# Optimization experiments

Measured on AMD Instinct MI355X. Metric: run time of the kernel, lower is better.

The kernel has to match this reference:

```python
import jax, jax.numpy as jnp
import numpy as np

NUM_STEPS = 2  # consensus iterations


def psi3(r, edge_index, W3, b3):
    # one-layer message passing GNN: sum-aggregate neighbors, add self, linear, relu
    src, dst = edge_index[0], edge_index[1]
    agg = jnp.zeros_like(r).at[dst].add(r[src])
    return jax.nn.relu((r + agg) @ W3 + b3)


def setup_inputs() -> dict:
    key = jax.random.key(0)
    ks = jax.random.split(key, 12)
    N_total, C_in = 4096, 128   # global entity table
    N_s, N_t = 1024, 1024       # source / target graph sizes (B=1)
    E = 16384                   # edges per graph (avg degree 16)
    C1, C2 = 256, 256           # psi_1 / psi_2 output dims
    R = 32                      # psi_3 in_channels == out_channels
    s_in = 1.0 / np.sqrt(C_in)
    s_r = 1.0 / np.sqrt(R)
    inp = {}
    inp['inputs'] = jax.random.normal(ks[0], (N_total, C_in), jnp.float32)
    inp['index_n1'] = jax.random.randint(ks[1], (N_s,), 0, N_total)
    inp['index_n2'] = jax.random.randint(ks[2], (N_t,), 0, N_total)
    inp['edge_index_s'] = jax.random.randint(ks[3], (2, E), 0, N_s)
    inp['edge_index_t'] = jax.random.randint(ks[4], (2, E), 0, N_t)
    # psi_1 / psi_2: linear entity encoders
    inp['W1'] = jax.random.uniform(ks[5], (C_in, C1), jnp.float32, -s_in, s_in)
    inp['W2'] = jax.random.uniform(ks[6], (C_in, C2), jnp.float32, -s_in, s_in)
    # psi_3 weights
    inp['W3'] = jax.random.uniform(ks[7], (R, R), jnp.float32, -s_r, s_r)
    inp['b3'] = jnp.zeros((R,), jnp.float32)
    # consensus MLP: R -> R -> 1
    inp['Wm1'] = jax.random.uniform(ks[8], (R, R), jnp.float32, -s_r, s_r)
    inp['bm1'] = jnp.zeros((R,), jnp.float32)
    inp['Wm2'] = jax.random.uniform(ks[9], (R, 1), jnp.float32, -s_r, s_r)
    inp['bm2'] = jnp.zeros((1,), jnp.float32)
    # random node indicator functions r_s for each consensus step (drawn
    # with torch.randn inside the original forward; precomputed here)
    inp['rs_all'] = jax.random.normal(ks[10], (NUM_STEPS, N_s, R), jnp.float32)
    return inp


def reference(inputs, index_n1, index_n2, edge_index_s, edge_index_t,
              W1, W2, W3, b3, Wm1, bm1, Wm2, bm2, rs_all):
    time_emb = inputs @ W1  # psi_1
    rel_emb = inputs @ W2   # psi_2
    # h = cat(time, rel) per node; B=1 so masks are all-true
    h_s = jnp.concatenate([time_emb[index_n1], rel_emb[index_n1]], axis=-1)  # [N_s, C1+C2]
    h_t = jnp.concatenate([time_emb[index_n2], rel_emb[index_n2]], axis=-1)  # [N_t, C1+C2]
    S_hat = h_s @ h_t.T  # [N_s, N_t] dense similarity
    S_0 = jax.nn.softmax(S_hat, axis=-1)  # masked_softmax with full mask

    def step(S_hat, r_s):
        S = jax.nn.softmax(S_hat, axis=-1)
        r_t = S.T @ r_s                                  # [N_t, R]
        o_s = psi3(r_s, edge_index_s, W3, b3)            # [N_s, R]
        o_t = psi3(r_t, edge_index_t, W3, b3)            # [N_t, R]
        D = o_s[:, None, :] - o_t[None, :, :]            # [N_s, N_t, R]
        delta = (jax.nn.relu(D @ Wm1 + bm1) @ Wm2 + bm2)[..., 0]  # mlp(D).squeeze(-1)
        return S_hat + delta, None

    S_hat, _ = jax.lax.scan(step, S_hat, rs_all)
    S_L = jax.nn.softmax(S_hat, axis=-1)
    return S_0, S_L
```

## Files before the change

### kernel.cpp

```cpp
#include <hip/hip_runtime.h>
#include <math.h>

#define N_S   1024
#define N_T   1024
#define C_IN  128
#define E_EDG 16384
#define R     32
#define NSTEP 2

__global__ __launch_bounds__(128) void k_gram(const float* __restrict__ W1,
                                              const float* __restrict__ W2,
                                              float* __restrict__ G) {
    int a = blockIdx.x;
    int b = threadIdx.x;
    __shared__ float wa[512];
    for (int c = threadIdx.x; c < 256; c += 128) {
        wa[c]       = W1[a * 256 + c];
        wa[256 + c] = W2[a * 256 + c];
    }
    __syncthreads();
    float acc = 0.f;
    for (int c = 0; c < 256; ++c)
        acc += wa[c] * W1[b * 256 + c] + wa[256 + c] * W2[b * 256 + c];
    G[a * 128 + b] = acc;
}

__global__ __launch_bounds__(128) void k_ys(const float* __restrict__ X,
                                            const int* __restrict__ idx1,
                                            const float* __restrict__ G,
                                            float* __restrict__ Ys) {
    int i = blockIdx.x;
    int a = threadIdx.x;
    __shared__ float x[128];
    int row = idx1[i];
    x[a] = X[row * 128 + a];
    __syncthreads();
    float acc = 0.f;
#pragma unroll 8
    for (int d = 0; d < 128; ++d)
        acc += x[d] * G[d * 128 + a];
    Ys[i * 128 + a] = acc;
}

__global__ __launch_bounds__(256) void k_shat(const float* __restrict__ Ys,
                                              const float* __restrict__ X,
                                              const int* __restrict__ idx2,
                                              float* __restrict__ Shat) {
    __shared__ float As[64][132];
    __shared__ float Bs[64][132];
    const int i0 = blockIdx.y * 64, j0 = blockIdx.x * 64;
    const int t = threadIdx.x;
    for (int s = t; s < 64 * 32; s += 256) {
        int row = s >> 5, q = s & 31;
        float4 v = ((const float4*)(Ys + (size_t)(i0 + row) * 128))[q];
        *(float4*)&As[row][q * 4] = v;
    }
    for (int s = t; s < 64 * 32; s += 256) {
        int row = s >> 5, q = s & 31;
        int src = idx2[j0 + row];
        float4 v = ((const float4*)(X + (size_t)src * 128))[q];
        *(float4*)&Bs[row][q * 4] = v;
    }
    __syncthreads();
    const int r = t >> 4, c = t & 15;
    float acc[4][4] = {};
    for (int k = 0; k < 128; k += 4) {
        float4 ya[4], xb[4];
#pragma unroll
        for (int a = 0; a < 4; ++a) ya[a] = *(const float4*)&As[r + 16 * a][k];
#pragma unroll
        for (int b = 0; b < 4; ++b) xb[b] = *(const float4*)&Bs[c + 16 * b][k];
#pragma unroll
        for (int a = 0; a < 4; ++a)
#pragma unroll
            for (int b = 0; b < 4; ++b)
                acc[a][b] += ya[a].x * xb[b].x + ya[a].y * xb[b].y +
                             ya[a].z * xb[b].z + ya[a].w * xb[b].w;
    }
#pragma unroll
    for (int a = 0; a < 4; ++a)
#pragma unroll
        for (int b = 0; b < 4; ++b)
            Shat[(size_t)(i0 + r + 16 * a) * 1024 + (j0 + c + 16 * b)] = acc[a][b];
}

__global__ __launch_bounds__(256) void k_softmax(const float* __restrict__ Shat,
                                                 float* __restrict__ Sdst,
                                                 float* __restrict__ out0) {
    int i = blockIdx.x;
    int t = threadIdx.x;
    const float* row = Shat + (size_t)i * 1024;
    float x[4];
#pragma unroll
    for (int j = 0; j < 4; ++j) x[j] = row[t + 256 * j];
    __shared__ float red[256];
    float m = fmaxf(fmaxf(x[0], x[1]), fmaxf(x[2], x[3]));
    red[t] = m;
    __syncthreads();
    for (int s = 128; s > 0; s >>= 1) {
        if (t < s) red[t] = fmaxf(red[t], red[t + s]);
        __syncthreads();
    }
    float rowmax = red[0];
    __syncthreads();
    float e[4], sum = 0.f;
#pragma unroll
    for (int j = 0; j < 4; ++j) { e[j] = expf(x[j] - rowmax); sum += e[j]; }
    red[t] = sum;
    __syncthreads();
    for (int s = 128; s > 0; s >>= 1) {
        if (t < s) red[t] += red[t + s];
        __syncthreads();
    }
    float inv = 1.f / red[0];
#pragma unroll
    for (int j = 0; j < 4; ++j) {
        float v = e[j] * inv;
        Sdst[(size_t)i * 1024 + t + 256 * j] = v;
        if (out0) out0[(size_t)i * 1024 + t + 256 * j] = v;
    }
}

__global__ __launch_bounds__(256) void k_rt(const float* __restrict__ S,
                                            const float* __restrict__ rs,
                                            float* __restrict__ rt) {
    int j0 = blockIdx.x * 64;
    int i0 = blockIdx.y * 128;
    int t = threadIdx.x;
    int k = t & 31;
    int jg = t >> 5;
    __shared__ float Sl[16][68];
    __shared__ float Rl[16][36];
    float acc[8] = {};
    for (int ic = 0; ic < 128; ic += 16) {
        for (int s = t; s < 16 * 16; s += 256) {
            int row = s >> 4, q = s & 15;
            *(float4*)&Sl[row][q * 4] =
                ((const float4*)(S + (size_t)(i0 + ic + row) * 1024 + j0))[q];
        }
        for (int s = t; s < 16 * 8; s += 256) {
            int row = s >> 3, q = s & 7;
            *(float4*)&Rl[row][q * 4] =
                ((const float4*)(rs + (size_t)(i0 + ic + row) * 32))[q];
        }
        __syncthreads();
#pragma unroll
        for (int ii = 0; ii < 16; ++ii) {
            float rv = Rl[ii][k];
#pragma unroll
            for (int m = 0; m < 8; ++m)
                acc[m] += Sl[ii][jg * 8 + m] * rv;
        }
        __syncthreads();
    }
#pragma unroll
    for (int m = 0; m < 8; ++m)
        atomicAdd(&rt[(size_t)(j0 + jg * 8 + m) * 32 + k], acc[m]);
}

__global__ __launch_bounds__(256) void k_scatter(const int* __restrict__ es,
                                                 const int* __restrict__ et,
                                                 const float* __restrict__ rs,
                                                 const float* __restrict__ rt,
                                                 float* __restrict__ aggs,
                                                 float* __restrict__ aggt) {
    int gid = blockIdx.x * 256 + threadIdx.x;
    int k = gid & 31;
    int e = gid >> 5;
    if (e < E_EDG) {
        int src = es[e], dst = es[E_EDG + e];
        atomicAdd(&aggs[(size_t)dst * 32 + k], rs[(size_t)src * 32 + k]);
    } else {
        e -= E_EDG;
        int src = et[e], dst = et[E_EDG + e];
        atomicAdd(&aggt[(size_t)dst * 32 + k], rt[(size_t)src * 32 + k]);
    }
}

__global__ __launch_bounds__(256) void k_post(const float* __restrict__ rs,
                                              const float* __restrict__ rt,
                                              const float* __restrict__ aggs,
                                              const float* __restrict__ aggt,
                                              const float* __restrict__ W3,
                                              const float* __restrict__ b3,
                                              const float* __restrict__ Wm1,
                                              const float* __restrict__ bm1,
                                              float* __restrict__ P,
                                              float* __restrict__ Q) {
    __shared__ float w3[1024], wm1[1024];
    __shared__ float ul[8][33], ol[8][33];
    int t = threadIdx.x;
    for (int s = t; s < 1024; s += 256) { w3[s] = W3[s]; wm1[s] = Wm1[s]; }
    int row8 = t >> 5, k = t & 31;
    int grow = blockIdx.x * 8 + row8;
    bool is_s = grow < 1024;
    int r = is_s ? grow : grow - 1024;
    const float* rin = is_s ? rs : rt;
    const float* agg = is_s ? aggs : aggt;
    ul[row8][k] = rin[(size_t)r * 32 + k] + agg[(size_t)r * 32 + k];
    __syncthreads();
    float acc = b3[k];
#pragma unroll
    for (int m = 0; m < 32; ++m) acc += ul[row8][m] * w3[m * 32 + k];
    ol[row8][k] = fmaxf(acc, 0.f);
    __syncthreads();
    float acc2 = is_s ? bm1[k] : 0.f;
#pragma unroll
    for (int m = 0; m < 32; ++m) acc2 += ol[row8][m] * wm1[m * 32 + k];
    if (is_s) P[(size_t)r * 32 + k] = acc2;
    else      Q[(size_t)r * 32 + k] = acc2;
}

__global__ __launch_bounds__(256) void k_delta(const float* __restrict__ P,
                                               const float* __restrict__ Q,
                                               const float* __restrict__ Wm2,
                                               const float* __restrict__ bm2,
                                               float* __restrict__ Shat) {
    __shared__ float Pl[64][36], Ql[64][36];
    int t = threadIdx.x;
    int i0 = blockIdx.y * 64, j0 = blockIdx.x * 64;
    for (int s = t; s < 64 * 8; s += 256) {
        int row = s >> 3, q = s & 7;
        *(float4*)&Pl[row][q * 4] = ((const float4*)(P + (size_t)(i0 + row) * 32))[q];
        *(float4*)&Ql[row][q * 4] = ((const float4*)(Q + (size_t)(j0 + row) * 32))[q];
    }
    __syncthreads();
    int r = t >> 4, c = t & 15;
    float bv = bm2[0];
    float acc[4][4] = {};
#pragma unroll
    for (int q = 0; q < 8; ++q) {
        float4 w = ((const float4*)Wm2)[q];
        float4 pa[4], qb[4];
#pragma unroll
        for (int a = 0; a < 4; ++a) pa[a] = *(const float4*)&Pl[r + 16 * a][q * 4];
#pragma unroll
        for (int b = 0; b < 4; ++b) qb[b] = *(const float4*)&Ql[c + 16 * b][q * 4];
#pragma unroll
        for (int a = 0; a < 4; ++a)
#pragma unroll
            for (int b = 0; b < 4; ++b)
                acc[a][b] += w.x * fmaxf(pa[a].x - qb[b].x, 0.f)
                           + w.y * fmaxf(pa[a].y - qb[b].y, 0.f)
                           + w.z * fmaxf(pa[a].z - qb[b].z, 0.f)
                           + w.w * fmaxf(pa[a].w - qb[b].w, 0.f);
    }
#pragma unroll
    for (int a = 0; a < 4; ++a)
#pragma unroll
        for (int b = 0; b < 4; ++b) {
            size_t idx = (size_t)(i0 + r + 16 * a) * 1024 + (j0 + c + 16 * b);
            Shat[idx] += acc[a][b] + bv;
        }
}

extern "C" void kernel_launch(void* const* d_in, const int* in_sizes, int n_in,
                              void* d_out, int out_size, void* d_ws, size_t ws_size,
                              hipStream_t stream) {
    const float* inputs = (const float*)d_in[0];
    const int*   idx1   = (const int*)d_in[1];
    const int*   idx2   = (const int*)d_in[2];
    const int*   es     = (const int*)d_in[3];
    const int*   et     = (const int*)d_in[4];
    const float* W1     = (const float*)d_in[5];
    const float* W2     = (const float*)d_in[6];
    const float* W3     = (const float*)d_in[7];
    const float* b3     = (const float*)d_in[8];
    const float* Wm1    = (const float*)d_in[9];
    const float* bm1    = (const float*)d_in[10];
    const float* Wm2    = (const float*)d_in[11];
    const float* bm2    = (const float*)d_in[12];
    const float* rs_all = (const float*)d_in[13];
    float* out = (float*)d_out;
    float* ws  = (float*)d_ws;

    float* Shat = ws;
    float* S    = Shat + (1 << 20);
    float* Ys   = S + (1 << 20);
    float* G    = Ys + 131072;
    float* rt   = G + 16384;
    float* aggs = rt + 32768;
    float* aggt = aggs + 32768;
    float* P    = aggt + 32768;
    float* Q    = P + 32768;

    k_gram<<<128, 128, 0, stream>>>(W1, W2, G);
    k_ys<<<1024, 128, 0, stream>>>(inputs, idx1, G, Ys);
    k_shat<<<dim3(16, 16), 256, 0, stream>>>(Ys, inputs, idx2, Shat);

    for (int step = 0; step < NSTEP; ++step) {
        const float* rs = rs_all + (size_t)step * N_S * R;
        hipMemsetAsync(rt, 0, 3 * 32768 * sizeof(float), stream);
        k_softmax<<<1024, 256, 0, stream>>>(Shat, S, step == 0 ? out : nullptr);
        k_rt<<<dim3(16, 8), 256, 0, stream>>>(S, rs, rt);
        k_scatter<<<4096, 256, 0, stream>>>(es, et, rs, rt, aggs, aggt);
        k_post<<<256, 256, 0, stream>>>(rs, rt, aggs, aggt, W3, b3, Wm1, bm1, P, Q);
        k_delta<<<dim3(16, 16), 256, 0, stream>>>(P, Q, Wm2, bm2, Shat);
    }
    k_softmax<<<1024, 256, 0, stream>>>(Shat, out + (1 << 20), nullptr);
}
```

Before: 182.8 us.

## Fuse softmax into GEMM epilogues via partial row stats and hoist source-side psi3

Removes the standalone softmax kernel. Per-tile row max and sum-of-exp partials are emitted in the S_hat and delta epilogues, and the normalization is applied on the fly while loading into the S^T·r_s product. The source-graph scatter and MLP projection for both steps are hoisted before the loop, since they do not depend on S. Memsets are replaced by zeroing inside k_pre and k_delta, and the Gram kernel gets a tiled, coalesced transpose. This cuts launches and full-matrix passes, at the cost of recomputing exp in k_rt and using the faster, less precise __expf.

```diff
diff --git a/kernel.cpp b/kernel.cpp
--- a/kernel.cpp
+++ b/kernel.cpp
@@ -8,21 +8,44 @@
 #define R     32
 #define NSTEP 2
 
-__global__ __launch_bounds__(128) void k_gram(const float* __restrict__ W1,
-                                              const float* __restrict__ W2,
-                                              float* __restrict__ G) {
+__global__ __launch_bounds__(256) void k_pre(const float* __restrict__ W1,
+                                             const float* __restrict__ W2,
+                                             float* __restrict__ G,
+                                             float* __restrict__ zbuf) {
+    int t = threadIdx.x;
+    ((float4*)zbuf)[blockIdx.x * 256 + t] = make_float4(0.f, 0.f, 0.f, 0.f);
+
     int a = blockIdx.x;
-    int b = threadIdx.x;
     __shared__ float wa[512];
-    for (int c = threadIdx.x; c < 256; c += 128) {
-        wa[c]       = W1[a * 256 + c];
-        wa[256 + c] = W2[a * 256 + c];
-    }
-    __syncthreads();
+    __shared__ float wt[64][129];
+    __shared__ float red[256];
+    for (int s = t; s < 512; s += 256)
+        wa[s] = (s < 256) ? W1[a * 256 + s] : W2[a * 256 + (s - 256)];
+    __syncthreads();
+
     float acc = 0.f;
-    for (int c = 0; c < 256; ++c)
-        acc += wa[c] * W1[b * 256 + c] + wa[256 + c] * W2[b * 256 + c];
-    G[a * 128 + b] = acc;
+    int b = t & 127, h = t >> 7;
+    for (int ci = 0; ci < 8; ++ci) {
+        const float* Wsrc = (ci < 4) ? W1 : W2;
+        int cbase = (ci < 4) ? ci * 64 : (ci - 4) * 64;
+#pragma unroll
+        for (int it = 0; it < 8; ++it) {
+            int s = it * 256 + t;
+            int br = s >> 4, q = s & 15;
+            float4 v = *(const float4*)(Wsrc + (size_t)br * 256 + cbase + q * 4);
+            wt[q * 4 + 0][br] = v.x; wt[q * 4 + 1][br] = v.y;
+            wt[q * 4 + 2][br] = v.z; wt[q * 4 + 3][br] = v.w;
+        }
+        __syncthreads();
+        const float* wac = wa + ci * 64 + h * 32;
+#pragma unroll
+        for (int cc = 0; cc < 32; ++cc)
+            acc += wac[cc] * wt[h * 32 + cc][b];
+        __syncthreads();
+    }
+    red[t] = acc;
+    __syncthreads();
+    if (t < 128) G[a * 128 + t] = red[t] + red[t + 128];
 }
 
 __global__ __launch_bounds__(128) void k_ys(const float* __restrict__ X,
@@ -45,7 +68,8 @@
 __global__ __launch_bounds__(256) void k_shat(const float* __restrict__ Ys,
                                               const float* __restrict__ X,
                                               const int* __restrict__ idx2,
-                                              float* __restrict__ Shat) {
+                                              float* __restrict__ Shat,
+                                              float2* __restrict__ part) {
     __shared__ float As[64][132];
     __shared__ float Bs[64][132];
     const int i0 = blockIdx.y * 64, j0 = blockIdx.x * 64;
@@ -78,65 +102,109 @@
                              ya[a].z * xb[b].z + ya[a].w * xb[b].w;
     }
 #pragma unroll
-    for (int a = 0; a < 4; ++a)
+    for (int a = 0; a < 4; ++a) {
 #pragma unroll
         for (int b = 0; b < 4; ++b)
             Shat[(size_t)(i0 + r + 16 * a) * 1024 + (j0 + c + 16 * b)] = acc[a][b];
-}
-
-__global__ __launch_bounds__(256) void k_softmax(const float* __restrict__ Shat,
-                                                 float* __restrict__ Sdst,
-                                                 float* __restrict__ out0) {
-    int i = blockIdx.x;
-    int t = threadIdx.x;
-    const float* row = Shat + (size_t)i * 1024;
-    float x[4];
-#pragma unroll
-    for (int j = 0; j < 4; ++j) x[j] = row[t + 256 * j];
-    __shared__ float red[256];
-    float m = fmaxf(fmaxf(x[0], x[1]), fmaxf(x[2], x[3]));
-    red[t] = m;
-    __syncthreads();
-    for (int s = 128; s > 0; s >>= 1) {
-        if (t < s) red[t] = fmaxf(red[t], red[t + s]);
-        __syncthreads();
-    }
-    float rowmax = red[0];
-    __syncthreads();
-    float e[4], sum = 0.f;
-#pragma unroll
-    for (int j = 0; j < 4; ++j) { e[j] = expf(x[j] - rowmax); sum += e[j]; }
-    red[t] = sum;
-    __syncthreads();
-    for (int s = 128; s > 0; s >>= 1) {
-        if (t < s) red[t] += red[t + s];
-        __syncthreads();
-    }
-    float inv = 1.f / red[0];
-#pragma unroll
-    for (int j = 0; j < 4; ++j) {
-        float v = e[j] * inv;
-        Sdst[(size_t)i * 1024 + t + 256 * j] = v;
-        if (out0) out0[(size_t)i * 1024 + t + 256 * j] = v;
-    }
-}
-
-__global__ __launch_bounds__(256) void k_rt(const float* __restrict__ S,
+        float M = fmaxf(fmaxf(acc[a][0], acc[a][1]), fmaxf(acc[a][2], acc[a][3]));
+#pragma unroll
+        for (int m = 1; m < 16; m <<= 1) M = fmaxf(M, __shfl_xor(M, m, 16));
+        float Ss = 0.f;
+#pragma unroll
+        for (int b = 0; b < 4; ++b) Ss += __expf(acc[a][b] - M);
+#pragma unroll
+        for (int m = 1; m < 16; m <<= 1) Ss += __shfl_xor(Ss, m, 16);
+        if (c == 0)
+            part[(size_t)(i0 + r + 16 * a) * 16 + blockIdx.x] = make_float2(M, Ss);
+    }
+}
+
+__global__ __launch_bounds__(256) void k_scat_s(const int* __restrict__ es,
+                                                const float* __restrict__ rs_all,
+                                                float* __restrict__ aggs0,
+                                                float* __restrict__ aggs1) {
+    int gid = blockIdx.x * 256 + threadIdx.x;
+    int k = gid & 31;
+    int ei = gid >> 5;
+    int step = ei >> 14;
+    int e = ei & (E_EDG - 1);
+    int src = es[e], dst = es[E_EDG + e];
+    const float* rs = rs_all + (size_t)step * N_S * R;
+    float* aggs = step ? aggs1 : aggs0;
+    atomicAdd(&aggs[(size_t)dst * 32 + k], rs[(size_t)src * 32 + k]);
+}
+
+__global__ __launch_bounds__(256) void k_post_s(const float* __restrict__ rs_all,
+                                                const float* __restrict__ aggs0,
+                                                const float* __restrict__ aggs1,
+                                                const float* __restrict__ W3,
+                                                const float* __restrict__ b3,
+                                                const float* __restrict__ Wm1,
+                                                const float* __restrict__ bm1,
+                                                float* __restrict__ P0,
+                                                float* __restrict__ P1) {
+    __shared__ float w3[1024], wm1[1024];
+    __shared__ float ul[8][33], ol[8][33];
+    int t = threadIdx.x;
+    for (int s = t; s < 1024; s += 256) { w3[s] = W3[s]; wm1[s] = Wm1[s]; }
+    int row8 = t >> 5, k = t & 31;
+    int grow = blockIdx.x * 8 + row8;
+    int step = grow >> 10;
+    int r = grow & 1023;
+    const float* rs = rs_all + (size_t)step * N_S * R;
+    const float* agg = step ? aggs1 : aggs0;
+    float* P = step ? P1 : P0;
+    ul[row8][k] = rs[(size_t)r * 32 + k] + agg[(size_t)r * 32 + k];
+    __syncthreads();
+    float acc = b3[k];
+#pragma unroll
+    for (int m = 0; m < 32; ++m) acc += ul[row8][m] * w3[m * 32 + k];
+    ol[row8][k] = fmaxf(acc, 0.f);
+    __syncthreads();
+    float acc2 = bm1[k];
+#pragma unroll
+    for (int m = 0; m < 32; ++m) acc2 += ol[row8][m] * wm1[m * 32 + k];
+    P[(size_t)r * 32 + k] = acc2;
+}
+
+__global__ __launch_bounds__(256) void k_rt(const float* __restrict__ Shat,
+                                            const float2* __restrict__ part,
                                             const float* __restrict__ rs,
-                                            float* __restrict__ rt) {
+                                            float* __restrict__ rt,
+                                            float* __restrict__ out0) {
     int j0 = blockIdx.x * 64;
     int i0 = blockIdx.y * 128;
     int t = threadIdx.x;
-    int k = t & 31;
-    int jg = t >> 5;
     __shared__ float Sl[16][68];
     __shared__ float Rl[16][36];
+    __shared__ float mrow[128], irow[128];
+    if (t < 128) {
+        const float2* pr = part + (size_t)(i0 + t) * 16;
+        float M = -1e30f, S = 0.f;
+        float2 ps[16];
+#pragma unroll
+        for (int q = 0; q < 16; ++q) { ps[q] = pr[q]; M = fmaxf(M, ps[q].x); }
+#pragma unroll
+        for (int q = 0; q < 16; ++q) S += ps[q].y * __expf(ps[q].x - M);
+        mrow[t] = M;
+        irow[t] = 1.f / S;
+    }
+    __syncthreads();
+    int k = t & 31, jg = t >> 5;
     float acc[8] = {};
     for (int ic = 0; ic < 128; ic += 16) {
         for (int s = t; s < 16 * 16; s += 256) {
             int row = s >> 4, q = s & 15;
-            *(float4*)&Sl[row][q * 4] =
-                ((const float4*)(S + (size_t)(i0 + ic + row) * 1024 + j0))[q];
+            int lr = ic + row;
+            float4 v = ((const float4*)(Shat + (size_t)(i0 + lr) * 1024 + j0))[q];
+            float m = mrow[lr], inv = irow[lr];
+            v.x = __expf(v.x - m) * inv;
+            v.y = __expf(v.y - m) * inv;
+            v.z = __expf(v.z - m) * inv;
+            v.w = __expf(v.w - m) * inv;
+            *(float4*)&Sl[row][q * 4] = v;
+            if (out0)
+                ((float4*)(out0 + (size_t)(i0 + lr) * 1024 + j0))[q] = v;
         }
         for (int s = t; s < 16 * 8; s += 256) {
             int row = s >> 3, q = s & 7;
@@ -158,66 +226,57 @@
         atomicAdd(&rt[(size_t)(j0 + jg * 8 + m) * 32 + k], acc[m]);
 }
 
-__global__ __launch_bounds__(256) void k_scatter(const int* __restrict__ es,
-                                                 const int* __restrict__ et,
-                                                 const float* __restrict__ rs,
-                                                 const float* __restrict__ rt,
-                                                 float* __restrict__ aggs,
-                                                 float* __restrict__ aggt) {
+__global__ __launch_bounds__(256) void k_scat_t(const int* __restrict__ et,
+                                                const float* __restrict__ rt,
+                                                float* __restrict__ aggt) {
     int gid = blockIdx.x * 256 + threadIdx.x;
     int k = gid & 31;
     int e = gid >> 5;
-    if (e < E_EDG) {
-        int src = es[e], dst = es[E_EDG + e];
-        atomicAdd(&aggs[(size_t)dst * 32 + k], rs[(size_t)src * 32 + k]);
-    } else {
-        e -= E_EDG;
-        int src = et[e], dst = et[E_EDG + e];
-        atomicAdd(&aggt[(size_t)dst * 32 + k], rt[(size_t)src * 32 + k]);
-    }
-}
-
-__global__ __launch_bounds__(256) void k_post(const float* __restrict__ rs,
-                                              const float* __restrict__ rt,
-                                              const float* __restrict__ aggs,
-                                              const float* __restrict__ aggt,
-                                              const float* __restrict__ W3,
-                                              const float* __restrict__ b3,
-                                              const float* __restrict__ Wm1,
-                                              const float* __restrict__ bm1,
-                                              float* __restrict__ P,
-                                              float* __restrict__ Q) {
+    int src = et[e], dst = et[E_EDG + e];
+    atomicAdd(&aggt[(size_t)dst * 32 + k], rt[(size_t)src * 32 + k]);
+}
+
+__global__ __launch_bounds__(256) void k_post_t(const float* __restrict__ rt,
+                                                const float* __restrict__ aggt,
+                                                const float* __restrict__ W3,
+                                                const float* __restrict__ b3,
+                                                const float* __restrict__ Wm1,
+                                                float* __restrict__ Q) {
     __shared__ float w3[1024], wm1[1024];
     __shared__ float ul[8][33], ol[8][33];
     int t = threadIdx.x;
     for (int s = t; s < 1024; s += 256) { w3[s] = W3[s]; wm1[s] = Wm1[s]; }
     int row8 = t >> 5, k = t & 31;
-    int grow = blockIdx.x * 8 + row8;
-    bool is_s = grow < 1024;
-    int r = is_s ? grow : grow - 1024;
-    const float* rin = is_s ? rs : rt;
-    const float* agg = is_s ? aggs : aggt;
-    ul[row8][k] = rin[(size_t)r * 32 + k] + agg[(size_t)r * 32 + k];
+    int r = blockIdx.x * 8 + row8;
+    ul[row8][k] = rt[(size_t)r * 32 + k] + aggt[(size_t)r * 32 + k];
     __syncthreads();
     float acc = b3[k];
 #pragma unroll
     for (int m = 0; m < 32; ++m) acc += ul[row8][m] * w3[m * 32 + k];
     ol[row8][k] = fmaxf(acc, 0.f);
     __syncthreads();
-    float acc2 = is_s ? bm1[k] : 0.f;
+    float acc2 = 0.f;
 #pragma unroll
     for (int m = 0; m < 32; ++m) acc2 += ol[row8][m] * wm1[m * 32 + k];
-    if (is_s) P[(size_t)r * 32 + k] = acc2;
-    else      Q[(size_t)r * 32 + k] = acc2;
+    Q[(size_t)r * 32 + k] = acc2;
 }
 
 __global__ __launch_bounds__(256) void k_delta(const float* __restrict__ P,
                                                const float* __restrict__ Q,
                                                const float* __restrict__ Wm2,
                                                const float* __restrict__ bm2,
-                                               float* __restrict__ Shat) {
+                                               float* __restrict__ Shat,
+                                               float2* __restrict__ part,
+                                               float* __restrict__ zbuf) {
     __shared__ float Pl[64][36], Ql[64][36];
     int t = threadIdx.x;
+    if (blockIdx.y == 0) {
+        float4 z = make_float4(0.f, 0.f, 0.f, 0.f);
+        float4* zb = (float4*)zbuf;
+        int base = (blockIdx.x * 256 + t) * 4;
+#pragma unroll
+        for (int q = 0; q < 4; ++q) zb[base + q] = z;
+    }
     int i0 = blockIdx.y * 64, j0 = blockIdx.x * 64;
     for (int s = t; s < 64 * 8; s += 256) {
         int row = s >> 3, q = s & 7;
@@ -246,12 +305,43 @@
                            + w.w * fmaxf(pa[a].w - qb[b].w, 0.f);
     }
 #pragma unroll
-    for (int a = 0; a < 4; ++a)
+    for (int a = 0; a < 4; ++a) {
+        float v[4];
 #pragma unroll
         for (int b = 0; b < 4; ++b) {
             size_t idx = (size_t)(i0 + r + 16 * a) * 1024 + (j0 + c + 16 * b);
-            Shat[idx] += acc[a][b] + bv;
-        }
+            v[b] = Shat[idx] + acc[a][b] + bv;
+            Shat[idx] = v[b];
+        }
+        float M = fmaxf(fmaxf(v[0], v[1]), fmaxf(v[2], v[3]));
+#pragma unroll
+        for (int m = 1; m < 16; m <<= 1) M = fmaxf(M, __shfl_xor(M, m, 16));
+        float Ss = 0.f;
+#pragma unroll
+        for (int b = 0; b < 4; ++b) Ss += __expf(v[b] - M);
+#pragma unroll
+        for (int m = 1; m < 16; m <<= 1) Ss += __shfl_xor(Ss, m, 16);
+        if (c == 0)
+            part[(size_t)(i0 + r + 16 * a) * 16 + blockIdx.x] = make_float2(M, Ss);
+    }
+}
+
+__global__ __launch_bounds__(256) void k_fsm(const float* __restrict__ Shat,
+                                             const float2* __restrict__ part,
+                                             float* __restrict__ out2) {
+    int i = blockIdx.x, t = threadIdx.x;
+    const float2* pr = part + (size_t)i * 16;
+    float M = -1e30f, S = 0.f;
+    float2 ps[16];
+#pragma unroll
+    for (int q = 0; q < 16; ++q) { ps[q] = pr[q]; M = fmaxf(M, ps[q].x); }
+#pragma unroll
+    for (int q = 0; q < 16; ++q) S += ps[q].y * __expf(ps[q].x - M);
+    float inv = 1.f / S;
+    const float* row = Shat + (size_t)i * 1024;
+#pragma unroll
+    for (int j = 0; j < 4; ++j)
+        out2[(size_t)i * 1024 + t + 256 * j] = __expf(row[t + 256 * j] - M) * inv;
 }
 
 extern "C" void kernel_launch(void* const* d_in, const int* in_sizes, int n_in,
@@ -274,28 +364,32 @@
     float* out = (float*)d_out;
     float* ws  = (float*)d_ws;
 
-    float* Shat = ws;
-    float* S    = Shat + (1 << 20);
-    float* Ys   = S + (1 << 20);
-    float* G    = Ys + 131072;
-    float* rt   = G + 16384;
-    float* aggs = rt + 32768;
-    float* aggt = aggs + 32768;
-    float* P    = aggt + 32768;
-    float* Q    = P + 32768;
-
-    k_gram<<<128, 128, 0, stream>>>(W1, W2, G);
+    float*  Shat  = ws;
+    float*  Ys    = Shat + (1 << 20);
+    float*  G     = Ys + 131072;
+    float2* part  = (float2*)(G + 16384);
+    float*  rt    = G + 16384 + 32768;
+    float*  aggt  = rt + 32768;
+    float*  aggs0 = aggt + 32768;
+    float*  aggs1 = aggs0 + 32768;
+    float*  P0    = aggs1 + 32768;
+    float*  P1    = P0 + 32768;
+    float*  Q     = P1 + 32768;
+
+    k_pre<<<128, 256, 0, stream>>>(W1, W2, G, rt);
     k_ys<<<1024, 128, 0, stream>>>(inputs, idx1, G, Ys);
-    k_shat<<<dim3(16, 16), 256, 0, stream>>>(Ys, inputs, idx2, Shat);
+    k_shat<<<dim3(16, 16), 256, 0, stream>>>(Ys, inputs, idx2, Shat, part);
+    k_scat_s<<<4096, 256, 0, stream>>>(es, rs_all, aggs0, aggs1);
+    k_post_s<<<256, 256, 0, stream>>>(rs_all, aggs0, aggs1, W3, b3, Wm1, bm1, P0, P1);
 
     for (int step = 0; step < NSTEP; ++step) {
         const float* rs = rs_all + (size_t)step * N_S * R;
-        hipMemsetAsync(rt, 0, 3 * 32768 * sizeof(float), stream);
-        k_softmax<<<1024, 256, 0, stream>>>(Shat, S, step == 0 ? out : nullptr);
-        k_rt<<<dim3(16, 8), 256, 0, stream>>>(S, rs, rt);
-        k_scatter<<<4096, 256, 0, stream>>>(es, et, rs, rt, aggs, aggt);
-        k_post<<<256, 256, 0, stream>>>(rs, rt, aggs, aggt, W3, b3, Wm1, bm1, P, Q);
-        k_delta<<<dim3(16, 16), 256, 0, stream>>>(P, Q, Wm2, bm2, Shat);
-    }
-    k_softmax<<<1024, 256, 0, stream>>>(Shat, out + (1 << 20), nullptr);
-}
+        k_rt<<<dim3(16, 8), 256, 0, stream>>>(Shat, part, rs, rt,
+                                              step == 0 ? out : nullptr);
+        k_scat_t<<<2048, 256, 0, stream>>>(et, rt, aggt);
+        k_post_t<<<128, 256, 0, stream>>>(rt, aggt, W3, b3, Wm1, Q);
+        k_delta<<<dim3(16, 16), 256, 0, stream>>>(step ? P1 : P0, Q, Wm2, bm2,
+                                                  Shat, part, rt);
+    }
+    k_fsm<<<1024, 256, 0, stream>>>(Shat, part, out + (1 << 20));
+}
```

After: 182.1 us. Within noise of the previous version (-0.4%).
